# Performance work log

Measured on AMD Instinct MI355X. Metric: run time of the kernel, lower is better.

The kernel has to match this reference:

```python
import jax, jax.numpy as jnp
import numpy as np

N_NODES = 50000
N_GRAPHS = 32
NODE_F = 16
GLOBAL_F = 2
HID = 300
LAT = 100
N_EDGES = 800000


def _glorot(key, shape):
    fan_in, fan_out = shape[0], shape[1]
    s = jnp.sqrt(2.0 / (fan_in + fan_out))
    return jax.random.normal(key, shape, dtype=jnp.float32) * s


def setup_inputs() -> dict:
    key = jax.random.key(0)
    ks = jax.random.split(key, 24)
    x = jax.random.normal(ks[0], (N_NODES, NODE_F), dtype=jnp.float32)
    edge_index = jax.random.randint(ks[1], (2, N_EDGES), 0, N_NODES, dtype=jnp.int64)
    batch = jnp.sort(jax.random.randint(ks[2], (N_NODES,), 0, N_GRAPHS, dtype=jnp.int64))
    u = jax.random.normal(ks[3], (N_GRAPHS, GLOBAL_F), dtype=jnp.float32)
    # layer 0: in=NODE_F, layer 1: in=LAT
    p = {}
    p['l0_w1'] = _glorot(ks[4], (2 * NODE_F, HID)); p['l0_b1'] = jnp.zeros((HID,), jnp.float32)
    p['l0_w2'] = _glorot(ks[5], (HID, HID));        p['l0_b2'] = jnp.zeros((HID,), jnp.float32)
    p['l0_w3'] = _glorot(ks[6], (HID, LAT));        p['l0_b3'] = jnp.zeros((LAT,), jnp.float32)
    p['l1_w1'] = _glorot(ks[7], (2 * LAT, HID));    p['l1_b1'] = jnp.zeros((HID,), jnp.float32)
    p['l1_w2'] = _glorot(ks[8], (HID, HID));        p['l1_b2'] = jnp.zeros((HID,), jnp.float32)
    p['l1_w3'] = _glorot(ks[9], (HID, LAT));        p['l1_b3'] = jnp.zeros((LAT,), jnp.float32)
    p['lin_w1'] = _glorot(ks[10], (LAT + GLOBAL_F, LAT)); p['lin_b1'] = jnp.zeros((LAT,), jnp.float32)
    p['lin_w2'] = _glorot(ks[11], (LAT, LAT));            p['lin_b2'] = jnp.zeros((LAT,), jnp.float32)
    p['lin_w3'] = _glorot(ks[12], (LAT, 1));              p['lin_b3'] = jnp.zeros((1,), jnp.float32)
    return dict(x=x, edge_index=edge_index, batch=batch, u=u, **p)


def _edge_layer(x, src, dst, w1, b1, w2, b2, w3, b3):
    # gather endpoints; torch_geometric default flow: x_j = x[src], x_i = x[dst]
    xi = x[dst]
    xj = x[src]
    inp = jnp.concatenate([xi, xj - xi], axis=-1)          # [E, 2*in]
    h = jax.nn.relu(inp @ w1 + b1)
    h = jax.nn.relu(h @ w2 + b2)
    m = h @ w3 + b3                                         # [E, out]
    s = jax.ops.segment_sum(m, dst, num_segments=N_NODES)  # scatter-sum to target nodes
    cnt = jax.ops.segment_sum(jnp.ones((m.shape[0],), m.dtype), dst, num_segments=N_NODES)
    return s / jnp.maximum(cnt, 1.0)[:, None]               # scatter-mean


def _mean_pool(x, batch):
    s = jax.ops.segment_sum(x, batch, num_segments=N_GRAPHS)
    cnt = jax.ops.segment_sum(jnp.ones((x.shape[0],), x.dtype), batch, num_segments=N_GRAPHS)
    return s / jnp.maximum(cnt, 1.0)[:, None]


def reference(x, edge_index, batch, u,
              l0_w1, l0_b1, l0_w2, l0_b2, l0_w3, l0_b3,
              l1_w1, l1_b1, l1_w2, l1_b2, l1_w3, l1_b3,
              lin_w1, lin_b1, lin_w2, lin_b2, lin_w3, lin_b3):
    src, dst = edge_index[0], edge_index[1]
    x = _edge_layer(x, src, dst, l0_w1, l0_b1, l0_w2, l0_b2, l0_w3, l0_b3)
    x = jax.nn.relu(x)
    x = _edge_layer(x, src, dst, l1_w1, l1_b1, l1_w2, l1_b2, l1_w3, l1_b3)
    x = jax.nn.relu(x)
    pooled = jnp.concatenate([_mean_pool(x, batch), u], axis=1)  # [G, LAT+GLOBAL_F]
    h = jax.nn.relu(pooled @ lin_w1 + lin_b1)
    h = jax.nn.relu(h @ lin_w2 + lin_b2)
    return h @ lin_w3 + lin_b3  # [G, 1]
```

## Files before the change

kernel.cpp:

```cpp
#include <hip/hip_runtime.h>
#include <cstdint>
#include <cstddef>

#define N_NODES  50000
#define N_GRAPHS 32
#define NODE_F   16
#define GLOBAL_F 2
#define HID      300
#define LAT      100
#define N_EDGES  800000

#define HIDP 320
#define LATP 128
#define NCT1 (HIDP/16)
#define NCT2 (LATP/16)
#define NKS  (HIDP/32)
#define EPB  64
#define ROWP 66

typedef __bf16 bf16x8 __attribute__((ext_vector_type(8)));
typedef float  f32x4  __attribute__((ext_vector_type(4)));

__device__ __forceinline__ float relu_f(float x){ return fmaxf(x, 0.f); }

__device__ __forceinline__ unsigned short f2bf(float x){
  unsigned int u = __float_as_uint(x);
  u = (u + 0x7FFFu + ((u >> 16) & 1u)) >> 16;
  return (unsigned short)u;
}
__device__ __forceinline__ unsigned short f2bf_hw(float x){
  __bf16 h = (__bf16)x;
  return __builtin_bit_cast(unsigned short, h);
}
__device__ __forceinline__ float bf2f(unsigned int h){
  return __uint_as_float(h << 16);
}

__global__ void zero_kernel(float* __restrict__ p, int n){
  int i = blockIdx.x*blockDim.x + threadIdx.x;
  if (i < n) p[i] = 0.f;
}

__global__ void hist_kernel(const int* __restrict__ ei, int* __restrict__ hist){
  int e = blockIdx.x*blockDim.x + threadIdx.x;
  if (e < N_EDGES) atomicAdd(&hist[ei[N_EDGES + e]], 1);
}

__global__ __launch_bounds__(256) void scan_kernel(const int* __restrict__ hist,
                                                   int* __restrict__ woff){
  __shared__ int part[256];
  const int t = threadIdx.x;
  const int CH = (N_NODES + 255) / 256;
  const int lo = t*CH, hi = (lo + CH < N_NODES) ? lo + CH : N_NODES;
  int s = 0;
  for (int i = lo; i < hi; ++i) s += hist[i];
  part[t] = s;
  __syncthreads();
  for (int d = 1; d < 256; d <<= 1){
    int v = (t >= d) ? part[t-d] : 0;
    __syncthreads();
    part[t] += v;
    __syncthreads();
  }
  int run = (t == 0) ? 0 : part[t-1];
  for (int i = lo; i < hi; ++i){ woff[i] = run; run += hist[i]; }
}

__global__ void sort_kernel(const int* __restrict__ ei, int* __restrict__ woff,
                            int* __restrict__ es, int* __restrict__ ed){
  int e = blockIdx.x*blockDim.x + threadIdx.x;
  if (e < N_EDGES){
    int s = ei[e], d = ei[N_EDGES + e];
    int pos = atomicAdd(&woff[d], 1);
    es[pos] = s; ed[pos] = d;
  }
}

__global__ void gstart_kernel(const int* __restrict__ batch, int* __restrict__ gstart){
  int n = blockIdx.x*blockDim.x + threadIdx.x;
  if (n < N_NODES){
    int b = batch[n];
    if (n == 0){ for (int g = 0; g <= b; ++g) gstart[g] = 0; }
    else {
      int bp = batch[n-1];
      for (int g = bp+1; g <= b; ++g) gstart[g] = n;
    }
    if (n == N_NODES-1){ for (int g = b+1; g <= N_GRAPHS; ++g) gstart[g] = N_NODES; }
  }
}

__global__ void pack_wfrag(const float* __restrict__ w, int K, int N, int nct,
                           unsigned short* __restrict__ out, int total){
  int i = blockIdx.x*blockDim.x + threadIdx.x;
  if (i >= total) return;
  int j  = i & 7;
  int l  = (i >> 3) & 63;
  int t  = i >> 9;
  int ct = t % nct, ks = t / nct;
  int n = ct*16 + (l & 15);
  int k = ks*32 + ((l >> 4) << 3) + j;
  float v = (k < K && n < N) ? w[(size_t)k*N + n] : 0.f;
  out[i] = f2bf(v);
}

template<int F>
__global__ void pack_w1frag(const float* __restrict__ w1,
                            unsigned short* __restrict__ out, int total){
  int i = blockIdx.x*blockDim.x + threadIdx.x;
  if (i >= total) return;
  int j  = i & 7;
  int l  = (i >> 3) & 63;
  int t  = i >> 9;
  int ct = t % 40, ks = t / 40;
  int n = ct*16 + (l & 15);
  int k = ks*32 + ((l >> 4) << 3) + j;
  float v = 0.f;
  if (k < F){
    if (n < HIDP){ if (n < HID) v = w1[(size_t)k*HID + n] - w1[(size_t)(F+k)*HID + n]; }
    else { int nn = n - HIDP; if (nn < HID) v = w1[(size_t)(F+k)*HID + nn]; }
  }
  out[i] = f2bf(v);
}

__global__ void pad_bias4(const float* __restrict__ a0, const float* __restrict__ a1,
                          const float* __restrict__ a2, const float* __restrict__ a3,
                          float* __restrict__ o0, float* __restrict__ o1,
                          float* __restrict__ o2, float* __restrict__ o3){
  int i = blockIdx.x*blockDim.x + threadIdx.x;
  if (i < HIDP){
    float v0 = (i < HID) ? a0[i] : 0.f;
    float v1 = (i < HID) ? a1[i] : 0.f;
    float v2 = (i < HID) ? a2[i] : 0.f;
    float v3 = (i < HID) ? a3[i] : 0.f;
    o0[i] = v0; o1[i] = v1; o2[i] = v2; o3[i] = v3;
  }
}

__global__ void cvt_x0(const float* __restrict__ x, unsigned short* __restrict__ xb){
  int i = blockIdx.x*blockDim.x + threadIdx.x;
  if (i < N_NODES*32){
    int n = i >> 5, c = i & 31;
    xb[i] = (c < NODE_F) ? f2bf(x[(size_t)n*NODE_F + c]) : 0;
  }
}

template<int KPAD>
__global__ __launch_bounds__(256) void node_gemm(
    const unsigned short* __restrict__ xb, const unsigned short* __restrict__ wf,
    unsigned short* __restrict__ Ub, unsigned short* __restrict__ Vb){
  constexpr int NCH = KPAD/8;
  __shared__ __align__(16) unsigned short at[NCH][ROWP][8];
  const int tid = threadIdx.x;
  const int n0 = blockIdx.x*64;
  for (int i = tid; i < 64*NCH; i += 256){
    int row = i / NCH, c = i % NCH;
    int n = n0 + row; if (n >= N_NODES) n = N_NODES-1;
    *(uint4*)&at[c][row][0] = *(const uint4*)&xb[(size_t)n*KPAD + c*8];
  }
  __syncthreads();
  const int wave = tid >> 6, l = tid & 63;
  const int lrow = l & 15, lq = l >> 4;
  f32x4 acc[4][10];
  #pragma unroll
  for (int rt = 0; rt < 4; ++rt)
    #pragma unroll
    for (int c = 0; c < 10; ++c)
      acc[rt][c] = (f32x4){0.f,0.f,0.f,0.f};
  for (int ks = 0; ks < KPAD/32; ++ks){
    bf16x8 a[4];
    #pragma unroll
    for (int rt = 0; rt < 4; ++rt)
      a[rt] = __builtin_bit_cast(bf16x8, *(const uint4*)&at[4*ks + lq][16*rt + lrow][0]);
    #pragma unroll
    for (int c = 0; c < 10; ++c){
      int ct = wave*10 + c;
      bf16x8 b = __builtin_bit_cast(bf16x8,
                   *(const uint4*)&wf[(((size_t)(ks*40 + ct)) << 9) + l*8]);
      #pragma unroll
      for (int rt = 0; rt < 4; ++rt)
        acc[rt][c] = __builtin_amdgcn_mfma_f32_16x16x32_bf16(a[rt], b, acc[rt][c], 0, 0, 0);
    }
  }
  #pragma unroll
  for (int c = 0; c < 10; ++c){
    int col = (wave*10 + c)*16 + lrow;
    #pragma unroll
    for (int rt = 0; rt < 4; ++rt){
      #pragma unroll
      for (int r = 0; r < 4; ++r){
        int n = n0 + rt*16 + lq*4 + r;
        if (n < N_NODES){
          unsigned short hv = f2bf_hw(acc[rt][c][r]);
          if (col < HIDP) Ub[(size_t)n*HIDP + col] = hv;
          else            Vb[(size_t)n*HIDP + col - HIDP] = hv;
        }
      }
    }
  }
}

__global__ __launch_bounds__(256, 3) void edge_mfma(
    const int* __restrict__ es, const int* __restrict__ ed,
    const unsigned short* __restrict__ U, const unsigned short* __restrict__ V,
    const float* __restrict__ b1p, const unsigned short* __restrict__ w2f,
    const float* __restrict__ b2p, const unsigned short* __restrict__ w3f,
    float* __restrict__ nodeacc){
  __shared__ __align__(16) unsigned short hs[HIDP/8][ROWP][8];
  __shared__ int sdst[EPB];
  const int tid = threadIdx.x;
  const int e0 = blockIdx.x * EPB;
  const int eL = tid & 63;
  const int mysrc = es[e0 + eL];
  const int mydst = ed[e0 + eL];
  if (tid < EPB) sdst[tid] = ed[e0 + tid];

  const size_t ubase = (size_t)mydst*HIDP;
  const size_t vbase = (size_t)mysrc*HIDP;
  #pragma unroll
  for (int it = 0; it < 10; ++it){
    int c = (tid + it*256) >> 6;
    const uint4 uu = *(const uint4*)&U[ubase + c*8];
    const uint4 vv = *(const uint4*)&V[vbase + c*8];
    const float4 bl = *(const float4*)&b1p[c*8];
    const float4 bh = *(const float4*)&b1p[c*8 + 4];
    const unsigned int uarr[4] = {uu.x, uu.y, uu.z, uu.w};
    const unsigned int varr[4] = {vv.x, vv.y, vv.z, vv.w};
    const float barr[8] = {bl.x, bl.y, bl.z, bl.w, bh.x, bh.y, bh.z, bh.w};
    unsigned int ou[4];
    #pragma unroll
    for (int q = 0; q < 4; ++q){
      float f0 = relu_f(bf2f(uarr[q] & 0xFFFFu) + bf2f(varr[q] & 0xFFFFu) + barr[2*q]);
      float f1 = relu_f(bf2f(uarr[q] >> 16)     + bf2f(varr[q] >> 16)     + barr[2*q+1]);
      ou[q] = (unsigned int)f2bf_hw(f0) | ((unsigned int)f2bf_hw(f1) << 16);
    }
    *(uint4*)&hs[c][eL][0] = make_uint4(ou[0], ou[1], ou[2], ou[3]);
  }
  __syncthreads();

  const int wave = tid >> 6, l = tid & 63;
  const int lrow = l & 15, lq = l >> 4;

  f32x4 acc1[4][5];
  #pragma unroll
  for (int rt = 0; rt < 4; ++rt)
    #pragma unroll
    for (int c = 0; c < 5; ++c)
      acc1[rt][c] = (f32x4){0.f,0.f,0.f,0.f};
  for (int ks = 0; ks < NKS; ++ks){
    bf16x8 a[4];
    #pragma unroll
    for (int rt = 0; rt < 4; ++rt)
      a[rt] = __builtin_bit_cast(bf16x8, *(const uint4*)&hs[4*ks + lq][16*rt + lrow][0]);
    #pragma unroll
    for (int c = 0; c < 5; ++c){
      int ct = wave*5 + c;
      bf16x8 b = __builtin_bit_cast(bf16x8,
                   *(const uint4*)&w2f[(((size_t)(ks*NCT1 + ct)) << 9) + l*8]);
      #pragma unroll
      for (int rt = 0; rt < 4; ++rt)
        acc1[rt][c] = __builtin_amdgcn_mfma_f32_16x16x32_bf16(a[rt], b, acc1[rt][c], 0, 0, 0);
    }
  }
  __syncthreads();

  #pragma unroll
  for (int c = 0; c < 5; ++c){
    int col = (wave*5 + c)*16 + lrow;
    float b2v = b2p[col];
    #pragma unroll
    for (int rt = 0; rt < 4; ++rt){
      #pragma unroll
      for (int r = 0; r < 4; ++r){
        int row = rt*16 + lq*4 + r;
        hs[col >> 3][row][col & 7] = f2bf_hw(relu_f(acc1[rt][c][r] + b2v));
      }
    }
  }
  __syncthreads();

  f32x4 acc2[4][2];
  #pragma unroll
  for (int rt = 0; rt < 4; ++rt)
    #pragma unroll
    for (int c = 0; c < 2; ++c)
      acc2[rt][c] = (f32x4){0.f,0.f,0.f,0.f};
  for (int ks = 0; ks < NKS; ++ks){
    bf16x8 a[4];
    #pragma unroll
    for (int rt = 0; rt < 4; ++rt)
      a[rt] = __builtin_bit_cast(bf16x8, *(const uint4*)&hs[4*ks + lq][16*rt + lrow][0]);
    #pragma unroll
    for (int c = 0; c < 2; ++c){
      int ct = wave*2 + c;
      bf16x8 b = __builtin_bit_cast(bf16x8,
                   *(const uint4*)&w3f[(((size_t)(ks*NCT2 + ct)) << 9) + l*8]);
      #pragma unroll
      for (int rt = 0; rt < 4; ++rt)
        acc2[rt][c] = __builtin_amdgcn_mfma_f32_16x16x32_bf16(a[rt], b, acc2[rt][c], 0, 0, 0);
    }
  }

  #pragma unroll
  for (int c = 0; c < 2; ++c){
    int col = (wave*2 + c)*16 + lrow;
    if (col < LAT){
      #pragma unroll
      for (int rt = 0; rt < 4; ++rt){
        int base = rt*16 + lq*4;
        int prev = sdst[base];
        float runv = acc2[rt][c][0];
        #pragma unroll
        for (int r = 1; r < 4; ++r){
          int d = sdst[base + r];
          float v = acc2[rt][c][r];
          if (d == prev) runv += v;
          else {
            atomicAdd(&nodeacc[(size_t)prev*LAT + col], runv);
            prev = d; runv = v;
          }
        }
        atomicAdd(&nodeacc[(size_t)prev*LAT + col], runv);
      }
    }
  }
}

__global__ void finalize_kernel(float* __restrict__ nodeacc, const int* __restrict__ hist,
                                const float* __restrict__ b3,
                                unsigned short* __restrict__ x1b){
  int idx = blockIdx.x*blockDim.x + threadIdx.x;
  if (idx < N_NODES*128){
    int n = idx >> 7, j = idx & 127;
    unsigned short o = 0;
    if (j < LAT){
      int c = hist[n];
      float v = nodeacc[(size_t)n*LAT + j] / fmaxf((float)c, 1.f);
      v += (c > 0) ? b3[j] : 0.f;
      o = f2bf_hw(relu_f(v));
      nodeacc[(size_t)n*LAT + j] = 0.f;
    }
    x1b[idx] = o;
  }
}

__global__ __launch_bounds__(512) void pool_seg(const unsigned short* __restrict__ x1b,
                                                const int* __restrict__ gstart,
                                                float* __restrict__ pooled){
  __shared__ float buf[3][128];
  const int g = blockIdx.x;
  const int lo = gstart[g], hi = gstart[g+1];
  const int col = threadIdx.x & 127, q = threadIdx.x >> 7;
  float s = 0.f;
  for (int n = lo + q; n < hi; n += 4) s += bf2f(x1b[(size_t)n*128 + col]);
  if (q) buf[q-1][col] = s;
  __syncthreads();
  if (q == 0 && col < LAT){
    float tot = s + buf[0][col] + buf[1][col] + buf[2][col];
    pooled[g*LAT + col] = tot / fmaxf((float)(hi - lo), 1.f);
  }
}

__global__ __launch_bounds__(128) void head_kernel(
    const float* __restrict__ pooled,
    const float* __restrict__ u,
    const float* __restrict__ w1, const float* __restrict__ bb1,
    const float* __restrict__ w2, const float* __restrict__ bb2,
    const float* __restrict__ w3, const float* __restrict__ bb3,
    float* __restrict__ out){
  __shared__ float p[N_GRAPHS][LAT+GLOBAL_F];
  __shared__ float h1[N_GRAPHS][LAT];
  __shared__ float h2[N_GRAPHS][LAT];
  const int tid = threadIdx.x;
  for (int t = tid; t < N_GRAPHS*LAT; t += 128){
    int g = t / LAT, k = t - g*LAT;
    p[g][k] = pooled[t];
  }
  for (int t = tid; t < N_GRAPHS*GLOBAL_F; t += 128){
    int g = t / GLOBAL_F, c = t - g*GLOBAL_F;
    p[g][LAT + c] = u[t];
  }
  __syncthreads();
  for (int t = tid; t < N_GRAPHS*LAT; t += 128){
    int g = t / LAT, j = t - g*LAT;
    float s = bb1[j];
    for (int k = 0; k < LAT+GLOBAL_F; k++) s += p[g][k]*w1[(size_t)k*LAT + j];
    h1[g][j] = relu_f(s);
  }
  __syncthreads();
  for (int t = tid; t < N_GRAPHS*LAT; t += 128){
    int g = t / LAT, j = t - g*LAT;
    float s = bb2[j];
    for (int k = 0; k < LAT; k++) s += h1[g][k]*w2[(size_t)k*LAT + j];
    h2[g][j] = relu_f(s);
  }
  __syncthreads();
  for (int t = tid; t < N_GRAPHS; t += 128){
    float s = bb3[0];
    for (int k = 0; k < LAT; k++) s += h2[t][k]*w3[k];
    out[t] = s;
  }
}

extern "C" void kernel_launch(void* const* d_in, const int* in_sizes, int n_in,
                              void* d_out, int out_size, void* d_ws, size_t ws_size,
                              hipStream_t stream){
  (void)in_sizes; (void)n_in; (void)out_size; (void)ws_size;
  const float* x     = (const float*)d_in[0];
  const int*   ei    = (const int*)d_in[1];
  const int*   batch = (const int*)d_in[2];
  const float* u     = (const float*)d_in[3];
  const float* l0_w1 = (const float*)d_in[4];  const float* l0_b1 = (const float*)d_in[5];
  const float* l0_w2 = (const float*)d_in[6];  const float* l0_b2 = (const float*)d_in[7];
  const float* l0_w3 = (const float*)d_in[8];  const float* l0_b3 = (const float*)d_in[9];
  const float* l1_w1 = (const float*)d_in[10]; const float* l1_b1 = (const float*)d_in[11];
  const float* l1_w2 = (const float*)d_in[12]; const float* l1_b2 = (const float*)d_in[13];
  const float* l1_w3 = (const float*)d_in[14]; const float* l1_b3 = (const float*)d_in[15];
  const float* lin_w1= (const float*)d_in[16]; const float* lin_b1= (const float*)d_in[17];
  const float* lin_w2= (const float*)d_in[18]; const float* lin_b2= (const float*)d_in[19];
  const float* lin_w3= (const float*)d_in[20]; const float* lin_b3= (const float*)d_in[21];

  char* wsb = (char*)d_ws;
  const size_t UV_BYTES  = (size_t)N_NODES*HIDP*sizeof(unsigned short);
  const size_t W2F_ELEMS = (size_t)NKS*NCT1*512;
  const size_t W3F_ELEMS = (size_t)NKS*NCT2*512;
  const size_t W1F0_ELEMS = (size_t)1*40*512;
  const size_t W1F1_ELEMS = (size_t)4*40*512;

  unsigned short* Ub   = (unsigned short*)wsb;  wsb += UV_BYTES;
  unsigned short* Vb   = (unsigned short*)wsb;  wsb += UV_BYTES;
  unsigned short* w2f0 = (unsigned short*)wsb;  wsb += W2F_ELEMS*2;
  unsigned short* w3f0 = (unsigned short*)wsb;  wsb += W3F_ELEMS*2;
  unsigned short* w2f1 = (unsigned short*)wsb;  wsb += W2F_ELEMS*2;
  unsigned short* w3f1 = (unsigned short*)wsb;  wsb += W3F_ELEMS*2;
  unsigned short* w1f0 = (unsigned short*)wsb;  wsb += W1F0_ELEMS*2;
  unsigned short* w1f1 = (unsigned short*)wsb;  wsb += W1F1_ELEMS*2;
  float* b1p0 = (float*)wsb;                    wsb += HIDP*4;
  float* b2p0 = (float*)wsb;                    wsb += HIDP*4;
  float* b1p1 = (float*)wsb;                    wsb += HIDP*4;
  float* b2p1 = (float*)wsb;                    wsb += HIDP*4;
  unsigned short* xb0 = (unsigned short*)wsb;   wsb += (size_t)N_NODES*32*2;
  unsigned short* x1b = (unsigned short*)wsb;   wsb += (size_t)N_NODES*128*2;
  float* nodeacc = (float*)wsb;                 wsb += (size_t)N_NODES*LAT*4;
  int*   hist    = (int*)wsb;                   wsb += (size_t)N_NODES*4;
  int*   woff    = (int*)wsb;                   wsb += (size_t)N_NODES*4;
  int*   es      = (int*)wsb;                   wsb += (size_t)N_EDGES*4;
  int*   ed      = (int*)wsb;                   wsb += (size_t)N_EDGES*4;
  int*   gstart  = (int*)wsb;                   wsb += 64*4;
  float* pooled  = (float*)wsb;                 wsb += (size_t)N_GRAPHS*LAT*4;

  {
    int zn = N_NODES*LAT + N_NODES;
    hipLaunchKernelGGL(zero_kernel, dim3((zn+255)/256), dim3(256), 0, stream, nodeacc, zn);
  }
  hipLaunchKernelGGL(hist_kernel, dim3((N_EDGES+255)/256), dim3(256), 0, stream, ei, hist);
  hipLaunchKernelGGL(scan_kernel, dim3(1), dim3(256), 0, stream, hist, woff);
  hipLaunchKernelGGL(sort_kernel, dim3((N_EDGES+255)/256), dim3(256), 0, stream,
                     ei, woff, es, ed);
  hipLaunchKernelGGL(gstart_kernel, dim3((N_NODES+255)/256), dim3(256), 0, stream,
                     batch, gstart);

  hipLaunchKernelGGL(pack_wfrag, dim3((W2F_ELEMS+255)/256), dim3(256), 0, stream,
                     l0_w2, HID, HID, NCT1, w2f0, (int)W2F_ELEMS);
  hipLaunchKernelGGL(pack_wfrag, dim3((W3F_ELEMS+255)/256), dim3(256), 0, stream,
                     l0_w3, HID, LAT, NCT2, w3f0, (int)W3F_ELEMS);
  hipLaunchKernelGGL(pack_wfrag, dim3((W2F_ELEMS+255)/256), dim3(256), 0, stream,
                     l1_w2, HID, HID, NCT1, w2f1, (int)W2F_ELEMS);
  hipLaunchKernelGGL(pack_wfrag, dim3((W3F_ELEMS+255)/256), dim3(256), 0, stream,
                     l1_w3, HID, LAT, NCT2, w3f1, (int)W3F_ELEMS);
  hipLaunchKernelGGL(pack_w1frag<NODE_F>, dim3((W1F0_ELEMS+255)/256), dim3(256), 0, stream,
                     l0_w1, w1f0, (int)W1F0_ELEMS);
  hipLaunchKernelGGL(pack_w1frag<LAT>, dim3((W1F1_ELEMS+255)/256), dim3(256), 0, stream,
                     l1_w1, w1f1, (int)W1F1_ELEMS);
  hipLaunchKernelGGL(pad_bias4, dim3(2), dim3(256), 0, stream,
                     l0_b1, l0_b2, l1_b1, l1_b2, b1p0, b2p0, b1p1, b2p1);
  hipLaunchKernelGGL(cvt_x0, dim3((N_NODES*32+255)/256), dim3(256), 0, stream, x, xb0);

  const int NGB = (N_NODES + 63)/64;

  hipLaunchKernelGGL(node_gemm<32>, dim3(NGB), dim3(256), 0, stream, xb0, w1f0, Ub, Vb);
  hipLaunchKernelGGL(edge_mfma, dim3(N_EDGES/EPB), dim3(256), 0, stream,
                     es, ed, Ub, Vb, b1p0, w2f0, b2p0, w3f0, nodeacc);
  hipLaunchKernelGGL(finalize_kernel, dim3((N_NODES*128+255)/256), dim3(256), 0, stream,
                     nodeacc, hist, l0_b3, x1b);

  hipLaunchKernelGGL(node_gemm<128>, dim3(NGB), dim3(256), 0, stream, x1b, w1f1, Ub, Vb);
  hipLaunchKernelGGL(edge_mfma, dim3(N_EDGES/EPB), dim3(256), 0, stream,
                     es, ed, Ub, Vb, b1p1, w2f1, b2p1, w3f1, nodeacc);
  hipLaunchKernelGGL(finalize_kernel, dim3((N_NODES*128+255)/256), dim3(256), 0, stream,
                     nodeacc, hist, l1_b3, x1b);

  hipLaunchKernelGGL(pool_seg, dim3(N_GRAPHS), dim3(512), 0, stream, x1b, gstart, pooled);
  hipLaunchKernelGGL(head_kernel, dim3(1), dim3(128), 0, stream,
                     pooled, u, lin_w1, lin_b1, lin_w2, lin_b2, lin_w3, lin_b3,
                     (float*)d_out);
}
```

Baseline: 1.547 ms.

## Enlarge edge tile to 96 edges and reduce scatter via shared-memory segments

```diff
diff --git a/kernel.cpp b/kernel.cpp
--- a/kernel.cpp
+++ b/kernel.cpp
@@ -15,8 +15,10 @@
 #define NCT1 (HIDP/16)
 #define NCT2 (LATP/16)
 #define NKS  (HIDP/32)
-#define EPB  64
-#define ROWP 66
+#define EPB  96
+#define NRT  6
+#define ROWP 98
+#define HSFS 132
 
 typedef __bf16 bf16x8 __attribute__((ext_vector_type(8)));
 typedef float  f32x4  __attribute__((ext_vector_type(4)));
@@ -89,10 +91,8 @@
   }
 }
 
-__global__ void pack_wfrag(const float* __restrict__ w, int K, int N, int nct,
-                           unsigned short* __restrict__ out, int total){
-  int i = blockIdx.x*blockDim.x + threadIdx.x;
-  if (i >= total) return;
+__device__ __forceinline__ void pack_one(const float* __restrict__ w, int K, int N,
+                                         int nct, unsigned short* __restrict__ out, int i){
   int j  = i & 7;
   int l  = (i >> 3) & 63;
   int t  = i >> 9;
@@ -101,6 +101,20 @@
   int k = ks*32 + ((l >> 4) << 3) + j;
   float v = (k < K && n < N) ? w[(size_t)k*N + n] : 0.f;
   out[i] = f2bf(v);
+}
+
+#define W2F_ELEMS (NKS*NCT1*512)
+#define W3F_ELEMS (NKS*NCT2*512)
+
+__global__ void pack_all(const float* __restrict__ w2a, const float* __restrict__ w3a,
+                         const float* __restrict__ w2b, const float* __restrict__ w3b,
+                         unsigned short* __restrict__ o2a, unsigned short* __restrict__ o3a,
+                         unsigned short* __restrict__ o2b, unsigned short* __restrict__ o3b){
+  int i = blockIdx.x*blockDim.x + threadIdx.x;
+  if (i < W2F_ELEMS) pack_one(w2a, HID, HID, NCT1, o2a, i);
+  else if (i < W2F_ELEMS + W3F_ELEMS) pack_one(w3a, HID, LAT, NCT2, o3a, i - W2F_ELEMS);
+  else if (i < 2*W2F_ELEMS + W3F_ELEMS) pack_one(w2b, HID, HID, NCT1, o2b, i - W2F_ELEMS - W3F_ELEMS);
+  else if (i < 2*W2F_ELEMS + 2*W3F_ELEMS) pack_one(w3b, HID, LAT, NCT2, o3b, i - 2*W2F_ELEMS - W3F_ELEMS);
 }
 
 template<int F>
@@ -128,11 +142,10 @@
                           float* __restrict__ o2, float* __restrict__ o3){
   int i = blockIdx.x*blockDim.x + threadIdx.x;
   if (i < HIDP){
-    float v0 = (i < HID) ? a0[i] : 0.f;
-    float v1 = (i < HID) ? a1[i] : 0.f;
-    float v2 = (i < HID) ? a2[i] : 0.f;
-    float v3 = (i < HID) ? a3[i] : 0.f;
-    o0[i] = v0; o1[i] = v1; o2[i] = v2; o3[i] = v3;
+    o0[i] = (i < HID) ? a0[i] : 0.f;
+    o1[i] = (i < HID) ? a1[i] : 0.f;
+    o2[i] = (i < HID) ? a2[i] : 0.f;
+    o3[i] = (i < HID) ? a3[i] : 0.f;
   }
 }
 
@@ -149,7 +162,7 @@
     const unsigned short* __restrict__ xb, const unsigned short* __restrict__ wf,
     unsigned short* __restrict__ Ub, unsigned short* __restrict__ Vb){
   constexpr int NCH = KPAD/8;
-  __shared__ __align__(16) unsigned short at[NCH][ROWP][8];
+  __shared__ __align__(16) unsigned short at[NCH][66][8];
   const int tid = threadIdx.x;
   const int n0 = blockIdx.x*64;
   for (int i = tid; i < 64*NCH; i += 256){
@@ -199,28 +212,33 @@
   }
 }
 
-__global__ __launch_bounds__(256, 3) void edge_mfma(
+__global__ __launch_bounds__(256, 2) void edge_mfma(
     const int* __restrict__ es, const int* __restrict__ ed,
     const unsigned short* __restrict__ U, const unsigned short* __restrict__ V,
     const float* __restrict__ b1p, const unsigned short* __restrict__ w2f,
     const float* __restrict__ b2p, const unsigned short* __restrict__ w3f,
     float* __restrict__ nodeacc){
-  __shared__ __align__(16) unsigned short hs[HIDP/8][ROWP][8];
+  __shared__ __align__(16) unsigned char smem[(HIDP/8)*ROWP*8*2];
   __shared__ int sdst[EPB];
+  __shared__ int sflag[EPB];
+  unsigned short* hsb = (unsigned short*)smem;
+  float*          hsf = (float*)smem;
+  #define HS(c,row) (hsb + (((c)*ROWP + (row)) << 3))
+
   const int tid = threadIdx.x;
   const int e0 = blockIdx.x * EPB;
-  const int eL = tid & 63;
-  const int mysrc = es[e0 + eL];
-  const int mydst = ed[e0 + eL];
-  if (tid < EPB) sdst[tid] = ed[e0 + tid];
-
-  const size_t ubase = (size_t)mydst*HIDP;
-  const size_t vbase = (size_t)mysrc*HIDP;
-  #pragma unroll
-  for (int it = 0; it < 10; ++it){
-    int c = (tid + it*256) >> 6;
-    const uint4 uu = *(const uint4*)&U[ubase + c*8];
-    const uint4 vv = *(const uint4*)&V[vbase + c*8];
+  const int nvalid = (N_EDGES - e0 < EPB) ? (N_EDGES - e0) : EPB;
+  if (tid < EPB) sdst[tid] = (tid < nvalid) ? ed[e0 + tid] : -1;
+
+  #pragma unroll
+  for (int it = 0; it < 15; ++it){
+    int idx = tid + it*256;
+    int e = idx / 40;
+    int c = idx - e*40;
+    int eg = e0 + e; if (eg >= N_EDGES) eg = N_EDGES - 1;
+    const int dn = ed[eg], sn = es[eg];
+    const uint4 uu = *(const uint4*)&U[(size_t)dn*HIDP + c*8];
+    const uint4 vv = *(const uint4*)&V[(size_t)sn*HIDP + c*8];
     const float4 bl = *(const float4*)&b1p[c*8];
     const float4 bh = *(const float4*)&b1p[c*8 + 4];
     const unsigned int uarr[4] = {uu.x, uu.y, uu.z, uu.w};
@@ -233,31 +251,31 @@
       float f1 = relu_f(bf2f(uarr[q] >> 16)     + bf2f(varr[q] >> 16)     + barr[2*q+1]);
       ou[q] = (unsigned int)f2bf_hw(f0) | ((unsigned int)f2bf_hw(f1) << 16);
     }
-    *(uint4*)&hs[c][eL][0] = make_uint4(ou[0], ou[1], ou[2], ou[3]);
+    *(uint4*)HS(c, e) = make_uint4(ou[0], ou[1], ou[2], ou[3]);
   }
   __syncthreads();
 
   const int wave = tid >> 6, l = tid & 63;
   const int lrow = l & 15, lq = l >> 4;
 
-  f32x4 acc1[4][5];
-  #pragma unroll
-  for (int rt = 0; rt < 4; ++rt)
+  f32x4 acc1[NRT][5];
+  #pragma unroll
+  for (int rt = 0; rt < NRT; ++rt)
     #pragma unroll
     for (int c = 0; c < 5; ++c)
       acc1[rt][c] = (f32x4){0.f,0.f,0.f,0.f};
   for (int ks = 0; ks < NKS; ++ks){
-    bf16x8 a[4];
-    #pragma unroll
-    for (int rt = 0; rt < 4; ++rt)
-      a[rt] = __builtin_bit_cast(bf16x8, *(const uint4*)&hs[4*ks + lq][16*rt + lrow][0]);
+    bf16x8 a[NRT];
+    #pragma unroll
+    for (int rt = 0; rt < NRT; ++rt)
+      a[rt] = __builtin_bit_cast(bf16x8, *(const uint4*)HS(4*ks + lq, 16*rt + lrow));
     #pragma unroll
     for (int c = 0; c < 5; ++c){
       int ct = wave*5 + c;
       bf16x8 b = __builtin_bit_cast(bf16x8,
                    *(const uint4*)&w2f[(((size_t)(ks*NCT1 + ct)) << 9) + l*8]);
       #pragma unroll
-      for (int rt = 0; rt < 4; ++rt)
+      for (int rt = 0; rt < NRT; ++rt)
         acc1[rt][c] = __builtin_amdgcn_mfma_f32_16x16x32_bf16(a[rt], b, acc1[rt][c], 0, 0, 0);
     }
   }
@@ -268,61 +286,69 @@
     int col = (wave*5 + c)*16 + lrow;
     float b2v = b2p[col];
     #pragma unroll
-    for (int rt = 0; rt < 4; ++rt){
+    for (int rt = 0; rt < NRT; ++rt){
       #pragma unroll
       for (int r = 0; r < 4; ++r){
         int row = rt*16 + lq*4 + r;
-        hs[col >> 3][row][col & 7] = f2bf_hw(relu_f(acc1[rt][c][r] + b2v));
+        HS(col >> 3, row)[col & 7] = f2bf_hw(relu_f(acc1[rt][c][r] + b2v));
       }
     }
   }
   __syncthreads();
 
-  f32x4 acc2[4][2];
-  #pragma unroll
-  for (int rt = 0; rt < 4; ++rt)
+  f32x4 acc2[NRT][2];
+  #pragma unroll
+  for (int rt = 0; rt < NRT; ++rt)
     #pragma unroll
     for (int c = 0; c < 2; ++c)
       acc2[rt][c] = (f32x4){0.f,0.f,0.f,0.f};
   for (int ks = 0; ks < NKS; ++ks){
-    bf16x8 a[4];
-    #pragma unroll
-    for (int rt = 0; rt < 4; ++rt)
-      a[rt] = __builtin_bit_cast(bf16x8, *(const uint4*)&hs[4*ks + lq][16*rt + lrow][0]);
+    bf16x8 a[NRT];
+    #pragma unroll
+    for (int rt = 0; rt < NRT; ++rt)
+      a[rt] = __builtin_bit_cast(bf16x8, *(const uint4*)HS(4*ks + lq, 16*rt + lrow));
     #pragma unroll
     for (int c = 0; c < 2; ++c){
       int ct = wave*2 + c;
       bf16x8 b = __builtin_bit_cast(bf16x8,
                    *(const uint4*)&w3f[(((size_t)(ks*NCT2 + ct)) << 9) + l*8]);
       #pragma unroll
-      for (int rt = 0; rt < 4; ++rt)
+      for (int rt = 0; rt < NRT; ++rt)
         acc2[rt][c] = __builtin_amdgcn_mfma_f32_16x16x32_bf16(a[rt], b, acc2[rt][c], 0, 0, 0);
     }
   }
+  __syncthreads();
 
   #pragma unroll
   for (int c = 0; c < 2; ++c){
     int col = (wave*2 + c)*16 + lrow;
+    #pragma unroll
+    for (int rt = 0; rt < NRT; ++rt){
+      #pragma unroll
+      for (int r = 0; r < 4; ++r){
+        int row = rt*16 + lq*4 + r;
+        hsf[row*HSFS + col] = acc2[rt][c][r];
+      }
+    }
+  }
+  if (tid < EPB) sflag[tid] = (tid == 0) || (sdst[tid] != sdst[tid-1]);
+  __syncthreads();
+
+  {
+    const int col = tid & 127;
     if (col < LAT){
-      #pragma unroll
-      for (int rt = 0; rt < 4; ++rt){
-        int base = rt*16 + lq*4;
-        int prev = sdst[base];
-        float runv = acc2[rt][c][0];
-        #pragma unroll
-        for (int r = 1; r < 4; ++r){
-          int d = sdst[base + r];
-          float v = acc2[rt][c][r];
-          if (d == prev) runv += v;
-          else {
-            atomicAdd(&nodeacc[(size_t)prev*LAT + col], runv);
-            prev = d; runv = v;
-          }
-        }
-        atomicAdd(&nodeacc[(size_t)prev*LAT + col], runv);
+      for (int s = tid >> 7; s < EPB; s += 2){
+        if (!sflag[s]) continue;
+        int d = sdst[s];
+        if (d < 0) continue;
+        float sum = hsf[s*HSFS + col];
+        int r = s + 1;
+        while (r < EPB && !sflag[r]){ sum += hsf[r*HSFS + col]; ++r; }
+        atomicAdd(&nodeacc[(size_t)d*LAT + col], sum);
       }
     }
   }
+  #undef HS
 }
 
 __global__ void finalize_kernel(float* __restrict__ nodeacc, const int* __restrict__ hist,
@@ -421,17 +447,15 @@
 
   char* wsb = (char*)d_ws;
   const size_t UV_BYTES  = (size_t)N_NODES*HIDP*sizeof(unsigned short);
-  const size_t W2F_ELEMS = (size_t)NKS*NCT1*512;
-  const size_t W3F_ELEMS = (size_t)NKS*NCT2*512;
   const size_t W1F0_ELEMS = (size_t)1*40*512;
   const size_t W1F1_ELEMS = (size_t)4*40*512;
 
   unsigned short* Ub   = (unsigned short*)wsb;  wsb += UV_BYTES;
   unsigned short* Vb   = (unsigned short*)wsb;  wsb += UV_BYTES;
-  unsigned short* w2f0 = (unsigned short*)wsb;  wsb += W2F_ELEMS*2;
-  unsigned short* w3f0 = (unsigned short*)wsb;  wsb += W3F_ELEMS*2;
-  unsigned short* w2f1 = (unsigned short*)wsb;  wsb += W2F_ELEMS*2;
-  unsigned short* w3f1 = (unsigned short*)wsb;  wsb += W3F_ELEMS*2;
+  unsigned short* w2f0 = (unsigned short*)wsb;  wsb += (size_t)W2F_ELEMS*2;
+  unsigned short* w3f0 = (unsigned short*)wsb;  wsb += (size_t)W3F_ELEMS*2;
+  unsigned short* w2f1 = (unsigned short*)wsb;  wsb += (size_t)W2F_ELEMS*2;
+  unsigned short* w3f1 = (unsigned short*)wsb;  wsb += (size_t)W3F_ELEMS*2;
   unsigned short* w1f0 = (unsigned short*)wsb;  wsb += W1F0_ELEMS*2;
   unsigned short* w1f1 = (unsigned short*)wsb;  wsb += W1F1_ELEMS*2;
   float* b1p0 = (float*)wsb;                    wsb += HIDP*4;
@@ -459,32 +483,30 @@
   hipLaunchKernelGGL(gstart_kernel, dim3((N_NODES+255)/256), dim3(256), 0, stream,
                      batch, gstart);
 
-  hipLaunchKernelGGL(pack_wfrag, dim3((W2F_ELEMS+255)/256), dim3(256), 0, stream,
-                     l0_w2, HID, HID, NCT1, w2f0, (int)W2F_ELEMS);
-  hipLaunchKernelGGL(pack_wfrag, dim3((W3F_ELEMS+255)/256), dim3(256), 0, stream,
-                     l0_w3, HID, LAT, NCT2, w3f0, (int)W3F_ELEMS);
-  hipLaunchKernelGGL(pack_wfrag, dim3((W2F_ELEMS+255)/256), dim3(256), 0, stream,
-                     l1_w2, HID, HID, NCT1, w2f1, (int)W2F_ELEMS);
-  hipLaunchKernelGGL(pack_wfrag, dim3((W3F_ELEMS+255)/256), dim3(256), 0, stream,
-                     l1_w3, HID, LAT, NCT2, w3f1, (int)W3F_ELEMS);
-  hipLaunchKernelGGL(pack_w1frag<NODE_F>, dim3((W1F0_ELEMS+255)/256), dim3(256), 0, stream,
+  {
+    int total = 2*W2F_ELEMS + 2*W3F_ELEMS;
+    hipLaunchKernelGGL(pack_all, dim3((total+255)/256), dim3(256), 0, stream,
+                       l0_w2, l0_w3, l1_w2, l1_w3, w2f0, w3f0, w2f1, w3f1);
+  }
+  hipLaunchKernelGGL(pack_w1frag<NODE_F>, dim3(((int)W1F0_ELEMS+255)/256), dim3(256), 0, stream,
                      l0_w1, w1f0, (int)W1F0_ELEMS);
-  hipLaunchKernelGGL(pack_w1frag<LAT>, dim3((W1F1_ELEMS+255)/256), dim3(256), 0, stream,
+  hipLaunchKernelGGL(pack_w1frag<LAT>, dim3(((int)W1F1_ELEMS+255)/256), dim3(256), 0, stream,
                      l1_w1, w1f1, (int)W1F1_ELEMS);
   hipLaunchKernelGGL(pad_bias4, dim3(2), dim3(256), 0, stream,
                      l0_b1, l0_b2, l1_b1, l1_b2, b1p0, b2p0, b1p1, b2p1);
   hipLaunchKernelGGL(cvt_x0, dim3((N_NODES*32+255)/256), dim3(256), 0, stream, x, xb0);
 
   const int NGB = (N_NODES + 63)/64;
+  const int NEB = (N_EDGES + EPB - 1)/EPB;
 
   hipLaunchKernelGGL(node_gemm<32>, dim3(NGB), dim3(256), 0, stream, xb0, w1f0, Ub, Vb);
-  hipLaunchKernelGGL(edge_mfma, dim3(N_EDGES/EPB), dim3(256), 0, stream,
+  hipLaunchKernelGGL(edge_mfma, dim3(NEB), dim3(256), 0, stream,
                      es, ed, Ub, Vb, b1p0, w2f0, b2p0, w3f0, nodeacc);
   hipLaunchKernelGGL(finalize_kernel, dim3((N_NODES*128+255)/256), dim3(256), 0, stream,
                      nodeacc, hist, l0_b3, x1b);
 
   hipLaunchKernelGGL(node_gemm<128>, dim3(NGB), dim3(256), 0, stream, x1b, w1f1, Ub, Vb);
-  hipLaunchKernelGGL(edge_mfma, dim3(N_EDGES/EPB), dim3(256), 0, stream,
+  hipLaunchKernelGGL(edge_mfma, dim3(NEB), dim3(256), 0, stream,
                      es, ed, Ub, Vb, b1p1, w2f1, b2p1, w3f1, nodeacc);
   hipLaunchKernelGGL(finalize_kernel, dim3((N_NODES*128+255)/256), dim3(256), 0, stream,
                      nodeacc, hist, l1_b3, x1b);
```

Result: slower. 1.637 ms (+5.9%).
